# Performance work log

Measured on AMD Instinct MI355X. Metric: run time of the kernel, lower is better.

Reference implementation:

```python
import jax, jax.numpy as jnp
import numpy as np

DIM = 768
NUM_HEADS = 12
HEAD_DIM = DIM // NUM_HEADS  # 64
H = W = 48


def setup_inputs() -> dict:
    key = jax.random.key(0)
    ks = jax.random.split(key, 7)
    x = jax.random.normal(ks[0], (2, H, W, DIM), dtype=jnp.float32)
    # qkv Linear: stored as [in, out] for x @ W convention
    qkv_w = jax.random.normal(ks[1], (DIM, 3 * DIM), dtype=jnp.float32) * (DIM ** -0.5)
    qkv_b = jax.random.normal(ks[2], (3 * DIM,), dtype=jnp.float32) * 0.02
    proj_w = jax.random.normal(ks[3], (DIM, DIM), dtype=jnp.float32) * (DIM ** -0.5)
    proj_b = jax.random.normal(ks[4], (DIM,), dtype=jnp.float32) * 0.02
    # decomposed relative position tables (trunc_normal std=0.02 ~ normal*0.02)
    rel_pos_h = jax.random.normal(ks[5], (2 * H - 1, HEAD_DIM), dtype=jnp.float32) * 0.02
    rel_pos_w = jax.random.normal(ks[6], (2 * W - 1, HEAD_DIM), dtype=jnp.float32) * 0.02
    return {"x": x, "qkv_w": qkv_w, "qkv_b": qkv_b, "proj_w": proj_w,
            "proj_b": proj_b, "rel_pos_h": rel_pos_h, "rel_pos_w": rel_pos_w}


def _get_rel_pos(size, rel_pos):
    # q_size == k_size == size; table already has 2*size-1 entries, no interp
    coords = jnp.arange(size)[:, None] - jnp.arange(size)[None, :] + (size - 1)
    return rel_pos[coords]  # [size, size, head_dim]


def reference(x, qkv_w, qkv_b, proj_w, proj_b, rel_pos_h, rel_pos_w):
    B, h, w, dim = x.shape
    nh, hd = NUM_HEADS, HEAD_DIM
    S = h * w
    scale = hd ** -0.5
    qkv = (x.reshape(B, S, dim) @ qkv_w + qkv_b).reshape(B, S, 3, nh, hd)
    qkv = jnp.transpose(qkv, (2, 0, 3, 1, 4)).reshape(3, B * nh, S, hd)
    q, k, v = qkv[0], qkv[1], qkv[2]
    attn = jnp.einsum("bqc,bkc->bqk", q * scale, k)  # [B*nh, S, S]
    # decomposed relative position bias
    Rh = _get_rel_pos(h, rel_pos_h)  # [h, h, hd]
    Rw = _get_rel_pos(w, rel_pos_w)  # [w, w, hd]
    r_q = q.reshape(B * nh, h, w, hd)
    rel_h = jnp.einsum("bhwc,hkc->bhwk", r_q, Rh)  # [B*nh, h, w, h]
    rel_w = jnp.einsum("bhwc,wkc->bhwk", r_q, Rw)  # [B*nh, h, w, w]
    attn = (attn.reshape(B * nh, h, w, h, w)
            + rel_h[:, :, :, :, None]
            + rel_w[:, :, :, None, :]).reshape(B * nh, S, S)
    attn = jax.nn.softmax(attn, axis=-1)
    out = (attn @ v).reshape(B, nh, h, w, hd)
    out = jnp.transpose(out, (0, 2, 3, 1, 4)).reshape(B, h, w, dim)
    return out @ proj_w + proj_b
```

## Files before the change

### kernel.cpp

```cpp
#include <hip/hip_runtime.h>
#include <hip/hip_fp16.h>

#define HD 64
#define SEQ 2304

typedef unsigned short u16;
typedef unsigned int u32;
using f32x4 = __attribute__((ext_vector_type(4))) float;
using s16x8 = __attribute__((ext_vector_type(8))) short;

static __device__ __forceinline__ float bf2f(u16 h) {
  union { float f; u32 u; } a; a.u = ((u32)h) << 16; return a.f;
}
static __device__ __forceinline__ void split2(float x, u16& h, u16& l) {
  u32 u = __float_as_uint(x);
  h = (u16)(u >> 16);
  float r = x - __uint_as_float(u & 0xffff0000u);
  l = (u16)(__float_as_uint(r) >> 16);
}
static __device__ __forceinline__ u16 rne_bf16(float x) {
  u32 u = __float_as_uint(x);
  return (u16)((u + 0x7fffu + ((u >> 16) & 1u)) >> 16);
}

__global__ __launch_bounds__(256) void conv_split_k(
    const float* __restrict__ src, u16* __restrict__ dhi, u16* __restrict__ dlo)
{
  const size_t i = ((size_t)blockIdx.x * 256 + threadIdx.x) * 8;
  f32x4 a = *(const f32x4*)(src + i);
  f32x4 b = *(const f32x4*)(src + i + 4);
  u16 h[8], l[8];
#pragma unroll
  for (int j = 0; j < 8; j++) {
    float x = j < 4 ? a[j] : b[j - 4];
    split2(x, h[j], l[j]);
  }
  *(uint4*)(dhi + i) = *(uint4*)&h[0];
  *(uint4*)(dlo + i) = *(uint4*)&l[0];
}

__global__ __launch_bounds__(256) void conv_wT_k(
    const float* __restrict__ src, u16* __restrict__ dhi, u16* __restrict__ dlo,
    int K, int N)
{
  __shared__ u32 t[64][65];
  const int tid = threadIdx.x;
  const int n0 = blockIdx.x * 64, k0 = blockIdx.y * 64;
  const int r = tid >> 2, c0 = (tid & 3) * 16;
  const float* sp = src + (size_t)(k0 + r) * N + n0 + c0;
#pragma unroll
  for (int j = 0; j < 16; j += 4) {
    f32x4 v = *(const f32x4*)(sp + j);
#pragma unroll
    for (int e = 0; e < 4; e++) {
      u16 h, l;
      split2(v[e], h, l);
      t[r][c0 + j + e] = (u32)h | ((u32)l << 16);
    }
  }
  __syncthreads();
  u16 hb[16], lb[16];
#pragma unroll
  for (int j = 0; j < 16; j++) {
    u32 p = t[c0 + j][r];
    hb[j] = (u16)(p & 0xffffu);
    lb[j] = (u16)(p >> 16);
  }
  size_t off = (size_t)(n0 + r) * K + k0 + c0;
  *(uint4*)(dhi + off)     = *(uint4*)&hb[0];
  *(uint4*)(dhi + off + 8) = *(uint4*)&hb[8];
  *(uint4*)(dlo + off)     = *(uint4*)&lb[0];
  *(uint4*)(dlo + off + 8) = *(uint4*)&lb[8];
}

static __device__ __forceinline__ void load16(
    const u16* pAh, const u16* pAl, const u16* pBh, const u16* pBl, int kk,
    s16x8 ah[4], s16x8 al[4], s16x8 bh[4], s16x8 bl[4])
{
#pragma unroll
  for (int mt = 0; mt < 4; mt++) {
    size_t o = (size_t)mt * 12288 + (size_t)kk * 32;
    ah[mt] = *(const s16x8*)(pAh + o);
    al[mt] = *(const s16x8*)(pAl + o);
    bh[mt] = *(const s16x8*)(pBh + o);
    bl[mt] = *(const s16x8*)(pBl + o);
  }
}
static __device__ __forceinline__ void mfma48(
    const s16x8 ah[4], const s16x8 al[4], const s16x8 bh[4], const s16x8 bl[4],
    f32x4 acc[4][4])
{
#pragma unroll
  for (int mt = 0; mt < 4; mt++)
#pragma unroll
    for (int nt = 0; nt < 4; nt++) {
      acc[mt][nt] = __builtin_amdgcn_mfma_f32_16x16x32_bf16(ah[mt], bh[nt], acc[mt][nt], 0, 0, 0);
      acc[mt][nt] = __builtin_amdgcn_mfma_f32_16x16x32_bf16(ah[mt], bl[nt], acc[mt][nt], 0, 0, 0);
      acc[mt][nt] = __builtin_amdgcn_mfma_f32_16x16x32_bf16(al[mt], bh[nt], acc[mt][nt], 0, 0, 0);
    }
}

__global__ __launch_bounds__(256, 2) void qkv_mfma_k(
    const u16* __restrict__ xhi, const u16* __restrict__ xlo,
    const u16* __restrict__ bthi, const u16* __restrict__ btlo,
    const float* __restrict__ bias,
    float* __restrict__ qbuf, u16* __restrict__ khi, u16* __restrict__ klo,
    u16* __restrict__ vhi)
{
  __shared__ __align__(16) u16 img[4][4096];
  const int tid = threadIdx.x;
  const int lane = tid & 63, wid = tid >> 6;
  const int g = lane >> 4, ql = lane & 15;
  const int wr = wid >> 1, wc = wid & 1;
  const int c0 = blockIdx.x * 128, r0 = blockIdx.y * 128;

  const u16* pAh = xhi  + (size_t)(r0 + wr * 64 + ql) * 768 + g * 8;
  const u16* pAl = xlo  + (size_t)(r0 + wr * 64 + ql) * 768 + g * 8;
  const u16* pBh = bthi + (size_t)(c0 + wc * 64 + ql) * 768 + g * 8;
  const u16* pBl = btlo + (size_t)(c0 + wc * 64 + ql) * 768 + g * 8;

  s16x8 Xah[4], Xal[4], Xbh[4], Xbl[4];
  s16x8 Yah[4], Yal[4], Ybh[4], Ybl[4];
  f32x4 acc[4][4] = {};

  load16(pAh, pAl, pBh, pBl, 0, Xah, Xal, Xbh, Xbl);
  for (int ks = 0; ks < 24; ks += 2) {
    load16(pAh, pAl, pBh, pBl, ks + 1, Yah, Yal, Ybh, Ybl);
    mfma48(Xah, Xal, Xbh, Xbl, acc);
    if (ks + 2 < 24)
      load16(pAh, pAl, pBh, pBl, ks + 2, Xah, Xal, Xbh, Xbl);
    mfma48(Yah, Yal, Ybh, Ybl, acc);
  }

  const int col0 = c0 + wc * 64;
  const int row0 = r0 + wr * 64;
  const int hb36 = col0 >> 6;
  const int which = hb36 / 12, head = hb36 - (hb36 / 12) * 12;
  const int b = row0 / 2304;
  const int sb = row0 - b * 2304;
  const int bh = b * 12 + head;
  float bb[4];
#pragma unroll
  for (int nt = 0; nt < 4; nt++) bb[nt] = bias[col0 + nt * 16 + ql];
#pragma unroll
  for (int mt = 0; mt < 4; mt++)
#pragma unroll
    for (int nt = 0; nt < 4; nt++)
#pragma unroll
      for (int r = 0; r < 4; r++)
        acc[mt][nt][r] += bb[nt];

  if (which == 0) {
#pragma unroll
    for (int mt = 0; mt < 4; mt++)
#pragma unroll
      for (int nt = 0; nt < 4; nt++)
#pragma unroll
        for (int r = 0; r < 4; r++) {
          int s = sb + mt * 16 + g * 4 + r;
          qbuf[((size_t)bh * SEQ + s) * 64 + nt * 16 + ql] = acc[mt][nt][r];
        }
  } else if (which == 1) {
    const int kt = sb >> 6;
    const size_t tile = ((size_t)bh * 36 + kt) * 4096;
    u16* const reg = img[wid];
#pragma unroll
    for (int mt = 0; mt < 4; mt++)
#pragma unroll
      for (int nt = 0; nt < 4; nt++) {
        int pcK = (nt >> 1) * 32 + (ql >> 2) * 8 + (nt & 1) * 4 + (ql & 3);
#pragma unroll
        for (int r = 0; r < 4; r++) {
          u16 h, l;
          split2(acc[mt][nt][r], h, l);
          reg[(mt * 16 + g * 4 + r) * 64 + pcK] = h;
        }
      }
    {
      const u16* src = reg + lane * 64;
      u16* dst = khi + tile + lane * 64;
#pragma unroll
      for (int j = 0; j < 8; j++)
        *(uint4*)(dst + j * 8) = *(const uint4*)(src + j * 8);
    }
#pragma unroll
    for (int mt = 0; mt < 4; mt++)
#pragma unroll
      for (int nt = 0; nt < 4; nt++) {
        int pcK = (nt >> 1) * 32 + (ql >> 2) * 8 + (nt & 1) * 4 + (ql & 3);
#pragma unroll
        for (int r = 0; r < 4; r++) {
          u16 h, l;
          split2(acc[mt][nt][r], h, l);
          reg[(mt * 16 + g * 4 + r) * 64 + pcK] = l;
        }
      }
    {
      const u16* src = reg + lane * 64;
      u16* dst = klo + tile + lane * 64;
#pragma unroll
      for (int j = 0; j < 8; j++)
        *(uint4*)(dst + j * 8) = *(const uint4*)(src + j * 8);
    }
  } else {
    const int kt = sb >> 6;
    const size_t tile = ((size_t)bh * 36 + kt) * 4096;
    u16* const reg = img[wid];
#pragma unroll
    for (int mt = 0; mt < 4; mt++)
#pragma unroll
      for (int nt = 0; nt < 4; nt++)
#pragma unroll
        for (int r = 0; r < 4; r++) {
          int off = (nt * 16 + ql) * 64 + (mt >> 1) * 32 + g * 8 + (mt & 1) * 4 + r;
          reg[off] = rne_bf16(acc[mt][nt][r]);
        }
    {
      const u16* src = reg + lane * 64;
      u16* dst = vhi + tile + lane * 64;
#pragma unroll
      for (int j = 0; j < 8; j++)
        *(uint4*)(dst + j * 8) = *(const uint4*)(src + j * 8);
    }
  }
}

#define BWS_OFF 18432
#define BH_OFF  27648
#define MS_OFF  (BH_OFF + 6372)
#define LS_OFF  (MS_OFF + 256)
__global__ __launch_bounds__(512) void attn_k(
    const float* __restrict__ qb,
    const u16* __restrict__ khi, const u16* __restrict__ klo,
    const u16* __restrict__ vhi,
    const float* __restrict__ rph, const float* __restrict__ rpw,
    u32* __restrict__ aop)
{
  __shared__ __align__(16) char pool[LS_OFF + 256];
  u16* KhiL = (u16*)pool;
  u16* KloL = (u16*)(pool + 9216);
  u16* VhL  = (u16*)(pool + 18432);
  __half* BwS = (__half*)(pool + BWS_OFF);
  __half* Bh  = (__half*)(pool + BH_OFF);
  float* m_s = (float*)(pool + MS_OFF);
  float* l_s = (float*)(pool + LS_OFF);
  float* qlds = (float*)pool;
  float* o_s  = (float*)pool;

  const int tid  = threadIdx.x;
  const int lane = tid & 63;
  const int wid  = tid >> 6;
  const int g    = lane >> 4;
  const int ql   = lane & 15;
  const int wq   = wid & 3;
  const int hh   = wid >> 2;
  const int bh   = blockIdx.x;
  const int qt   = blockIdx.y;
  const int s0   = qt * 64;

  {
    int row = tid >> 3, c0 = (tid & 7) * 8;
    const float* src = qb + ((size_t)bh * SEQ + s0 + row) * HD + c0;
    f32x4 v0 = *(const f32x4*)src;
    f32x4 v1 = *(const f32x4*)(src + 4);
    *(f32x4*)&qlds[row * 68 + c0]     = v0;
    *(f32x4*)&qlds[row * 68 + c0 + 4] = v1;
  }
  __syncthreads();

  s16x8 qfh[2], qfl[2];
  {
    int qrow = wq * 16 + ql;
#pragma unroll
    for (int ds = 0; ds < 2; ds++) {
#pragma unroll
      for (int h2 = 0; h2 < 2; h2++) {
        f32x4 qv = *(const f32x4*)&qlds[qrow * 68 + g * 4 + h2 * 16 + ds * 32];
#pragma unroll
        for (int j = 0; j < 4; j++) {
          u16 hi, lo;
          split2(qv[j], hi, lo);
          qfh[ds][h2 * 4 + j] = (short)hi;
          qfl[ds][h2 * 4 + j] = (short)lo;
        }
      }
    }
  }

  const size_t tbK = (size_t)bh * 36 * 4096;
  const int srow = tid >> 3;
  const int sch  = ((tid & 7) - (srow & 7)) & 7;
  const size_t soff = (size_t)srow * 64 + sch * 8;
  uint4 rkh = *(const uint4*)(khi + tbK + soff);
  uint4 rkl = *(const uint4*)(klo + tbK + soff);
  uint4 rvh = *(const uint4*)(vhi + tbK + soff);

  for (int i = tid; i < 64 * 96; i += 512) {
    int q = i / 96, j = i - (i / 96) * 96;
    int s = s0 + q;
    int qhg = s / 48, qw = s - qhg * 48;
    const float* tab;
    int ridx, col;
    if (j < 48) { col = j;      ridx = qhg - j + 47;        tab = rph; }
    else        { col = j - 48; ridx = qw - (j - 48) + 47;  tab = rpw; }
    const float* rp = tab + (size_t)ridx * HD;
    const float* qp = &qlds[q * 68];
    float s1 = 0.f;
#pragma unroll 4
    for (int d = 0; d < 64; d += 4) {
      f32x4 a = *(const f32x4*)(qp + d);
      f32x4 bv = *(const f32x4*)(rp + d);
      s1 += a[0]*bv[0] + a[1]*bv[1] + a[2]*bv[2] + a[3]*bv[3];
    }
    if (j < 48) Bh[col * 65 + q] = __float2half_rn(s1);
    else        BwS[col * 65 + q] = __float2half_rn(s1);
  }
  __syncthreads();

  const int q64b = wq * 16 + ql;

  float wA[4], wB[4], wC[4];
  {
    float b0[4], b1[4], b2[4];
#pragma unroll
    for (int r = 0; r < 4; r++) {
      b0[r] = __half2float(BwS[(      g * 4 + r) * 65 + q64b]);
      b1[r] = __half2float(BwS[(16 +  g * 4 + r) * 65 + q64b]);
      b2[r] = __half2float(BwS[(32 +  g * 4 + r) * 65 + q64b]);
    }
#pragma unroll
    for (int r = 0; r < 4; r++) {
      wA[r] = hh ? b2[r] : b0[r];
      wB[r] = hh ? b0[r] : b1[r];
      wC[r] = hh ? b1[r] : b2[r];
    }
  }

  float m_r = -3.0e38f, l_r = 0.f;
  f32x4 oacc[4] = {};

#define ATTN_TILE(KT, WA_, WB_, WRAP1) {                                        \
    const int kt = (KT);                                                        \
    __syncthreads();                                                            \
    *(uint4*)(KhiL + srow * 72 + sch * 8) = rkh;                                \
    *(uint4*)(KloL + srow * 72 + sch * 8) = rkl;                                \
    *(uint4*)(VhL  + srow * 72 + sch * 8) = rvh;                                \
    __syncthreads();                                                            \
    if (kt < 35) {                                                              \
      size_t tb = tbK + (size_t)(kt + 1) * 4096;                                \
      rkh = *(const uint4*)(khi + tb + soff);                                   \
      rkl = *(const uint4*)(klo + tb + soff);                                   \
      rvh = *(const uint4*)(vhi + tb + soff);                                   \
    }                                                                           \
    f32x4 sacc[2] = {};                                                         \
    _Pragma("unroll")                                                           \
    for (int ds = 0; ds < 2; ds++) {                                            \
      _Pragma("unroll")                                                         \
      for (int t2 = 0; t2 < 2; t2++) {                                          \
        int row = (hh * 2 + t2) * 16 + ql;                                      \
        s16x8 af = *(const s16x8*)(KhiL + row * 72 + ds * 32 + g * 8);          \
        s16x8 al = *(const s16x8*)(KloL + row * 72 + ds * 32 + g * 8);          \
        sacc[t2] = __builtin_amdgcn_mfma_f32_16x16x32_bf16(af, qfh[ds], sacc[t2], 0, 0, 0); \
        sacc[t2] = __builtin_amdgcn_mfma_f32_16x16x32_bf16(af, qfl[ds], sacc[t2], 0, 0, 0); \
        sacc[t2] = __builtin_amdgcn_mfma_f32_16x16x32_bf16(al, qfh[ds], sacc[t2], 0, 0, 0); \
      }                                                                         \
    }                                                                           \
    u32 kg0 = (u32)(kt * 64 + hh * 32);                                         \
    u32 kh0 = kg0 / 48u;                                                        \
    float bh0v = __half2float(Bh[kh0 * 65 + q64b]);                             \
    float bh1v = __half2float(Bh[(kh0 + 1) * 65 + q64b]);                       \
    float bhB = (WRAP1) ? bh1v : bh0v;                                          \
    float lg[8];                                                                \
    float tmax = -3.0e38f;                                                      \
    _Pragma("unroll")                                                           \
    for (int r = 0; r < 4; r++) {                                               \
      float x0 = sacc[0][r] * 0.125f + (bh0v + WA_[r]);                         \
      float x1 = sacc[1][r] * 0.125f + (bhB  + WB_[r]);                         \
      lg[r]     = x0;                                                           \
      lg[4 + r] = x1;                                                           \
      tmax = fmaxf(tmax, fmaxf(x0, x1));                                        \
    }                                                                           \
    tmax = fmaxf(tmax, __shfl_xor(tmax, 16));                                   \
    tmax = fmaxf(tmax, __shfl_xor(tmax, 32));                                   \
    if (__any(tmax > m_r + 6.0f)) {                                             \
      float mnew = fmaxf(m_r, tmax);                                            \
      float corr = __expf(m_r - mnew);                                          \
      l_r *= corr;                                                              \
      m_r = mnew;                                                               \
      float cq[4];                                                              \
      _Pragma("unroll")                                                         \
      for (int r = 0; r < 4; r++) cq[r] = __shfl(corr, g * 4 + r);              \
      _Pragma("unroll")                                                         \
      for (int dt = 0; dt < 4; dt++)                                            \
        _Pragma("unroll")                                                       \
        for (int r = 0; r < 4; r++) oacc[dt][r] *= cq[r];                       \
    }                                                                           \
    float psum = 0.f;                                                           \
    s16x8 pfh;                                                                  \
    _Pragma("unroll")                                                           \
    for (int j = 0; j < 8; j++) {                                               \
      float p = __expf(lg[j] - m_r);                                            \
      psum += p;                                                                \
      pfh[j] = (short)(u16)(__float_as_uint(p) >> 16);                          \
    }                                                                           \
    l_r += psum;                                                                \
    _Pragma("unroll")                                                           \
    for (int dt = 0; dt < 4; dt++) {                                            \
      int row = ql + 16 * dt;                                                   \
      s16x8 bhf = *(const s16x8*)(VhL + row * 72 + hh * 32 + g * 8);            \
      oacc[dt] = __builtin_amdgcn_mfma_f32_16x16x32_bf16(pfh, bhf, oacc[dt], 0, 0, 0); \
    }                                                                           \
  }

  for (int kt0 = 0; kt0 < 36; kt0 += 3) {
    ATTN_TILE(kt0 + 0, wA, wB, hh != 0);
    ATTN_TILE(kt0 + 1, wB, wC, false);
    ATTN_TILE(kt0 + 2, wC, wA, hh == 0);
  }
#undef ATTN_TILE

  l_r += __shfl_xor(l_r, 16);
  l_r += __shfl_xor(l_r, 32);

  __syncthreads();
  if (hh == 1) {
    if (g == 0) { m_s[q64b] = m_r; l_s[q64b] = l_r; }
#pragma unroll
    for (int dt = 0; dt < 4; dt++)
#pragma unroll
      for (int r = 0; r < 4; r++)
        o_s[(wq * 16 + g * 4 + r) * 68 + ql + 16 * dt] = oacc[dt][r];
  }
  __syncthreads();
  if (hh == 0) {
    float m2 = m_s[q64b];
    float l2 = l_s[q64b];
    float mf = fmaxf(m_r, m2);
    float c1 = __expf(m_r - mf);
    float c2 = __expf(m2 - mf);
    float lf = l_r * c1 + l2 * c2;
    float c1q[4], c2q[4], lfq[4];
#pragma unroll
    for (int r = 0; r < 4; r++) {
      c1q[r] = __shfl(c1, g * 4 + r);
      c2q[r] = __shfl(c2, g * 4 + r);
      lfq[r] = __shfl(lf, g * 4 + r);
    }
    const int b = bh / 12, head = bh - (bh / 12) * 12;
#pragma unroll
    for (int dt = 0; dt < 4; dt++)
#pragma unroll
      for (int r = 0; r < 4; r++) {
        float oo = oacc[dt][r] * c1q[r]
                 + o_s[(wq * 16 + g * 4 + r) * 68 + ql + 16 * dt] * c2q[r];
        float on = oo / lfq[r];
        int s = s0 + wq * 16 + g * 4 + r;
        size_t idx = ((size_t)b * SEQ + s) * 768 + head * 64 + ql + 16 * dt;
        u16 h, l;
        split2(on, h, l);
        aop[idx] = (u32)h | ((u32)l << 16);
      }
  }
}

static __device__ __forceinline__ void unpack8(
    const uint4 w0, const uint4 w1, s16x8& h, s16x8& l)
{
  u32 w[8];
  *(uint4*)&w[0] = w0; *(uint4*)&w[4] = w1;
  u32 hw[4], lw[4];
#pragma unroll
  for (int i = 0; i < 4; i++) {
    hw[i] = (w[2*i] & 0xffffu) | (w[2*i+1] << 16);
    lw[i] = (w[2*i] >> 16) | (w[2*i+1] & 0xffff0000u);
  }
  h = *(s16x8*)&hw[0];
  l = *(s16x8*)&lw[0];
}
static __device__ __forceinline__ void loadP(
    const u32* pA, const u16* pBh, const u16* pBl, int kk,
    uint4 aw[4][2], s16x8 bh[4], s16x8 bl[4])
{
#pragma unroll
  for (int mt = 0; mt < 4; mt++) {
    size_t oa = (size_t)mt * 12288 + (size_t)kk * 32;
    aw[mt][0] = *(const uint4*)(pA + oa);
    aw[mt][1] = *(const uint4*)(pA + oa + 4);
    size_t ob = (size_t)mt * 12288 + (size_t)kk * 32;
    bh[mt] = *(const s16x8*)(pBh + ob);
    bl[mt] = *(const s16x8*)(pBl + ob);
  }
}
static __device__ __forceinline__ void mfmaP(
    uint4 aw[4][2], const s16x8 bh[4], const s16x8 bl[4], f32x4 acc[4][4])
{
#pragma unroll
  for (int mt = 0; mt < 4; mt++) {
    s16x8 ah, al;
    unpack8(aw[mt][0], aw[mt][1], ah, al);
#pragma unroll
    for (int nt = 0; nt < 4; nt++) {
      acc[mt][nt] = __builtin_amdgcn_mfma_f32_16x16x32_bf16(ah, bh[nt], acc[mt][nt], 0, 0, 0);
      acc[mt][nt] = __builtin_amdgcn_mfma_f32_16x16x32_bf16(ah, bl[nt], acc[mt][nt], 0, 0, 0);
      acc[mt][nt] = __builtin_amdgcn_mfma_f32_16x16x32_bf16(al, bh[nt], acc[mt][nt], 0, 0, 0);
    }
  }
}

__global__ __launch_bounds__(256, 2) void proj_mfma_k(
    const u32* __restrict__ aop,
    const u16* __restrict__ bthi, const u16* __restrict__ btlo,
    const float* __restrict__ bias, float* __restrict__ out)
{
  const int tid = threadIdx.x;
  const int lane = tid & 63, wid = tid >> 6;
  const int g = lane >> 4, ql = lane & 15;
  const int wr = wid >> 1, wc = wid & 1;
  const int c0 = blockIdx.x * 128, r0 = blockIdx.y * 128;

  const u32* pA  = aop  + (size_t)(r0 + wr * 64 + ql) * 768 + g * 8;
  const u16* pBh = bthi + (size_t)(c0 + wc * 64 + ql) * 768 + g * 8;
  const u16* pBl = btlo + (size_t)(c0 + wc * 64 + ql) * 768 + g * 8;

  uint4 Xa[4][2]; s16x8 Xbh[4], Xbl[4];
  uint4 Ya[4][2]; s16x8 Ybh[4], Ybl[4];
  f32x4 acc[4][4] = {};

  loadP(pA, pBh, pBl, 0, Xa, Xbh, Xbl);
  for (int ks = 0; ks < 24; ks += 2) {
    loadP(pA, pBh, pBl, ks + 1, Ya, Ybh, Ybl);
    mfmaP(Xa, Xbh, Xbl, acc);
    if (ks + 2 < 24)
      loadP(pA, pBh, pBl, ks + 2, Xa, Xbh, Xbl);
    mfmaP(Ya, Ybh, Ybl, acc);
  }

  const int col0 = c0 + wc * 64;
  const int row0 = r0 + wr * 64;
  float bb[4];
#pragma unroll
  for (int nt = 0; nt < 4; nt++) bb[nt] = bias[col0 + nt * 16 + ql];
#pragma unroll
  for (int mt = 0; mt < 4; mt++)
#pragma unroll
    for (int nt = 0; nt < 4; nt++)
#pragma unroll
      for (int r = 0; r < 4; r++)
        out[(size_t)(row0 + mt * 16 + g * 4 + r) * 768 + col0 + nt * 16 + ql] =
            acc[mt][nt][r] + bb[nt];
}

extern "C" void kernel_launch(void* const* d_in, const int* in_sizes, int n_in,
                              void* d_out, int out_size, void* d_ws, size_t ws_size,
                              hipStream_t stream) {
  const float* x      = (const float*)d_in[0];
  const float* qkv_w  = (const float*)d_in[1];
  const float* qkv_b  = (const float*)d_in[2];
  const float* proj_w = (const float*)d_in[3];
  const float* proj_b = (const float*)d_in[4];
  const float* rph    = (const float*)d_in[5];
  const float* rpw    = (const float*)d_in[6];
  float* out = (float*)d_out;
  float* ws  = (float*)d_ws;

  const size_t SZ = (size_t)24 * SEQ * HD;
  float* qbuf = ws;
  u16* khi = (u16*)(ws + SZ);
  u16* klo = khi + SZ;
  u16* vhi = klo + SZ;
  u16* xhi = (u16*)(ws + 3 * SZ);
  u16* xlo = xhi + SZ;
  u32* aop = (u32*)(ws + 4 * SZ);
  u16* wqThi = (u16*)(ws + 5 * SZ);
  u16* wqTlo = wqThi + 768 * 2304;
  u16* wpThi = wqTlo + 768 * 2304;
  u16* wpTlo = wpThi + 768 * 768;

  conv_split_k<<<1728, 256, 0, stream>>>(x, xhi, xlo);
  conv_wT_k <<<dim3(36, 12), 256, 0, stream>>>(qkv_w, wqThi, wqTlo, 768, 2304);
  conv_wT_k <<<dim3(12, 12), 256, 0, stream>>>(proj_w, wpThi, wpTlo, 768, 768);
  qkv_mfma_k<<<dim3(18, 36), 256, 0, stream>>>(xhi, xlo, wqThi, wqTlo, qkv_b,
                                               qbuf, khi, klo, vhi);
  attn_k    <<<dim3(24, 36), 512, 0, stream>>>(qbuf, khi, klo, vhi, rph, rpw, aop);
  proj_mfma_k<<<dim3(6, 36), 256, 0, stream>>>(aop, wpThi, wpTlo, proj_b, out);
}
```

Before: 454.2 us.

## Fuse x bf16 split into QKV GEMM and merge weight-transpose kernels

The standalone kernel that split x into bf16 hi/lo arrays is removed. The QKV GEMM now loads fp32 x directly and performs the hi/lo split in registers just before the MFMAs. The two weight-transpose launches are merged into a single grid that picks the source matrix per block. This removes one full pass over x, its intermediate buffers and two launches, at the cost of reading twice the A bytes (fp32) inside the GEMM and adding split ALU work in the inner loop.

Result: no change. 446.5 us, median of 2 (-1.7%).

```diff
diff --git a/kernel.cpp b/kernel.cpp
--- a/kernel.cpp
+++ b/kernel.cpp
@@ -23,29 +23,20 @@
   return (u16)((u + 0x7fffu + ((u >> 16) & 1u)) >> 16);
 }
 
-__global__ __launch_bounds__(256) void conv_split_k(
-    const float* __restrict__ src, u16* __restrict__ dhi, u16* __restrict__ dlo)
-{
-  const size_t i = ((size_t)blockIdx.x * 256 + threadIdx.x) * 8;
-  f32x4 a = *(const f32x4*)(src + i);
-  f32x4 b = *(const f32x4*)(src + i + 4);
-  u16 h[8], l[8];
-#pragma unroll
-  for (int j = 0; j < 8; j++) {
-    float x = j < 4 ? a[j] : b[j - 4];
-    split2(x, h[j], l[j]);
-  }
-  *(uint4*)(dhi + i) = *(uint4*)&h[0];
-  *(uint4*)(dlo + i) = *(uint4*)&l[0];
-}
-
-__global__ __launch_bounds__(256) void conv_wT_k(
-    const float* __restrict__ src, u16* __restrict__ dhi, u16* __restrict__ dlo,
-    int K, int N)
+__global__ __launch_bounds__(256) void conv_wT2_k(
+    const float* __restrict__ wq, const float* __restrict__ wp,
+    u16* __restrict__ qhiT, u16* __restrict__ qloT,
+    u16* __restrict__ phiT, u16* __restrict__ ploT)
 {
   __shared__ u32 t[64][65];
   const int tid = threadIdx.x;
-  const int n0 = blockIdx.x * 64, k0 = blockIdx.y * 64;
+  const bool isq = blockIdx.x < 36;
+  const int bx = isq ? blockIdx.x : blockIdx.x - 36;
+  const float* src = isq ? wq : wp;
+  u16* dhi = isq ? qhiT : phiT;
+  u16* dlo = isq ? qloT : ploT;
+  const int N = isq ? 2304 : 768;
+  const int n0 = bx * 64, k0 = blockIdx.y * 64;
   const int r = tid >> 2, c0 = (tid & 3) * 16;
   const float* sp = src + (size_t)(k0 + r) * N + n0 + c0;
 #pragma unroll
@@ -66,42 +57,50 @@
     hb[j] = (u16)(p & 0xffffu);
     lb[j] = (u16)(p >> 16);
   }
-  size_t off = (size_t)(n0 + r) * K + k0 + c0;
+  size_t off = (size_t)(n0 + r) * 768 + k0 + c0;
   *(uint4*)(dhi + off)     = *(uint4*)&hb[0];
   *(uint4*)(dhi + off + 8) = *(uint4*)&hb[8];
   *(uint4*)(dlo + off)     = *(uint4*)&lb[0];
   *(uint4*)(dlo + off + 8) = *(uint4*)&lb[8];
 }
 
-static __device__ __forceinline__ void load16(
-    const u16* pAh, const u16* pAl, const u16* pBh, const u16* pBl, int kk,
-    s16x8 ah[4], s16x8 al[4], s16x8 bh[4], s16x8 bl[4])
+static __device__ __forceinline__ void loadF(
+    const float* pA, const u16* pBh, const u16* pBl, int kk,
+    uint4 aw[4][2], s16x8 bh[4], s16x8 bl[4])
 {
 #pragma unroll
   for (int mt = 0; mt < 4; mt++) {
     size_t o = (size_t)mt * 12288 + (size_t)kk * 32;
-    ah[mt] = *(const s16x8*)(pAh + o);
-    al[mt] = *(const s16x8*)(pAl + o);
+    aw[mt][0] = *(const uint4*)(pA + o);
+    aw[mt][1] = *(const uint4*)(pA + o + 4);
     bh[mt] = *(const s16x8*)(pBh + o);
     bl[mt] = *(const s16x8*)(pBl + o);
   }
 }
-static __device__ __forceinline__ void mfma48(
-    const s16x8 ah[4], const s16x8 al[4], const s16x8 bh[4], const s16x8 bl[4],
-    f32x4 acc[4][4])
-{
-#pragma unroll
-  for (int mt = 0; mt < 4; mt++)
+static __device__ __forceinline__ void mfmaF(
+    uint4 aw[4][2], const s16x8 bh[4], const s16x8 bl[4], f32x4 acc[4][4])
+{
+#pragma unroll
+  for (int mt = 0; mt < 4; mt++) {
+    u32 w[8];
+    *(uint4*)&w[0] = aw[mt][0]; *(uint4*)&w[4] = aw[mt][1];
+    u16 hh[8], ll[8];
+#pragma unroll
+    for (int j = 0; j < 8; j++)
+      split2(__uint_as_float(w[j]), hh[j], ll[j]);
+    s16x8 ah = *(s16x8*)&hh[0];
+    s16x8 al = *(s16x8*)&ll[0];
 #pragma unroll
     for (int nt = 0; nt < 4; nt++) {
-      acc[mt][nt] = __builtin_amdgcn_mfma_f32_16x16x32_bf16(ah[mt], bh[nt], acc[mt][nt], 0, 0, 0);
-      acc[mt][nt] = __builtin_amdgcn_mfma_f32_16x16x32_bf16(ah[mt], bl[nt], acc[mt][nt], 0, 0, 0);
-      acc[mt][nt] = __builtin_amdgcn_mfma_f32_16x16x32_bf16(al[mt], bh[nt], acc[mt][nt], 0, 0, 0);
-    }
+      acc[mt][nt] = __builtin_amdgcn_mfma_f32_16x16x32_bf16(ah, bh[nt], acc[mt][nt], 0, 0, 0);
+      acc[mt][nt] = __builtin_amdgcn_mfma_f32_16x16x32_bf16(ah, bl[nt], acc[mt][nt], 0, 0, 0);
+      acc[mt][nt] = __builtin_amdgcn_mfma_f32_16x16x32_bf16(al, bh[nt], acc[mt][nt], 0, 0, 0);
+    }
+  }
 }
 
 __global__ __launch_bounds__(256, 2) void qkv_mfma_k(
-    const u16* __restrict__ xhi, const u16* __restrict__ xlo,
+    const float* __restrict__ x,
     const u16* __restrict__ bthi, const u16* __restrict__ btlo,
     const float* __restrict__ bias,
     float* __restrict__ qbuf, u16* __restrict__ khi, u16* __restrict__ klo,
@@ -114,22 +113,21 @@
   const int wr = wid >> 1, wc = wid & 1;
   const int c0 = blockIdx.x * 128, r0 = blockIdx.y * 128;
 
-  const u16* pAh = xhi  + (size_t)(r0 + wr * 64 + ql) * 768 + g * 8;
-  const u16* pAl = xlo  + (size_t)(r0 + wr * 64 + ql) * 768 + g * 8;
+  const float* pA = x    + (size_t)(r0 + wr * 64 + ql) * 768 + g * 8;
   const u16* pBh = bthi + (size_t)(c0 + wc * 64 + ql) * 768 + g * 8;
   const u16* pBl = btlo + (size_t)(c0 + wc * 64 + ql) * 768 + g * 8;
 
-  s16x8 Xah[4], Xal[4], Xbh[4], Xbl[4];
-  s16x8 Yah[4], Yal[4], Ybh[4], Ybl[4];
+  uint4 Xa[4][2]; s16x8 Xbh[4], Xbl[4];
+  uint4 Ya[4][2]; s16x8 Ybh[4], Ybl[4];
   f32x4 acc[4][4] = {};
 
-  load16(pAh, pAl, pBh, pBl, 0, Xah, Xal, Xbh, Xbl);
+  loadF(pA, pBh, pBl, 0, Xa, Xbh, Xbl);
   for (int ks = 0; ks < 24; ks += 2) {
-    load16(pAh, pAl, pBh, pBl, ks + 1, Yah, Yal, Ybh, Ybl);
-    mfma48(Xah, Xal, Xbh, Xbl, acc);
+    loadF(pA, pBh, pBl, ks + 1, Ya, Ybh, Ybl);
+    mfmaF(Xa, Xbh, Xbl, acc);
     if (ks + 2 < 24)
-      load16(pAh, pAl, pBh, pBl, ks + 2, Xah, Xal, Xbh, Xbl);
-    mfma48(Yah, Yal, Ybh, Ybl, acc);
+      loadF(pA, pBh, pBl, ks + 2, Xa, Xbh, Xbl);
+    mfmaF(Ya, Ybh, Ybl, acc);
   }
 
   const int col0 = c0 + wc * 64;
@@ -568,19 +566,16 @@
   u16* khi = (u16*)(ws + SZ);
   u16* klo = khi + SZ;
   u16* vhi = klo + SZ;
-  u16* xhi = (u16*)(ws + 3 * SZ);
-  u16* xlo = xhi + SZ;
   u32* aop = (u32*)(ws + 4 * SZ);
   u16* wqThi = (u16*)(ws + 5 * SZ);
   u16* wqTlo = wqThi + 768 * 2304;
   u16* wpThi = wqTlo + 768 * 2304;
   u16* wpTlo = wpThi + 768 * 768;
 
-  conv_split_k<<<1728, 256, 0, stream>>>(x, xhi, xlo);
-  conv_wT_k <<<dim3(36, 12), 256, 0, stream>>>(qkv_w, wqThi, wqTlo, 768, 2304);
-  conv_wT_k <<<dim3(12, 12), 256, 0, stream>>>(proj_w, wpThi, wpTlo, 768, 768);
-  qkv_mfma_k<<<dim3(18, 36), 256, 0, stream>>>(xhi, xlo, wqThi, wqTlo, qkv_b,
-                                               qbuf, khi, klo, vhi);
-  attn_k    <<<dim3(24, 36), 512, 0, stream>>>(qbuf, khi, klo, vhi, rph, rpw, aop);
+  conv_wT2_k <<<dim3(48, 12), 256, 0, stream>>>(qkv_w, proj_w,
+                                                wqThi, wqTlo, wpThi, wpTlo);
+  qkv_mfma_k <<<dim3(18, 36), 256, 0, stream>>>(x, wqThi, wqTlo, qkv_b,
+                                                qbuf, khi, klo, vhi);
+  attn_k     <<<dim3(24, 36), 512, 0, stream>>>(qbuf, khi, klo, vhi, rph, rpw, aop);
   proj_mfma_k<<<dim3(6, 36), 256, 0, stream>>>(aop, wpThi, wpTlo, proj_b, out);
 }
```
